# Performance work log

Hardware: AMD Instinct MI355X
Metric: run time of the kernel (lower is better)

The kernel has to match this reference:

```python
import jax, jax.numpy as jnp
import numpy as np

N_TYPES = 4
AEV_DIM = 384
HIDDEN = [160, 128, 96]
CELU_ALPHA = 0.1


def _init_params(key):
    dims = [AEV_DIM] + HIDDEN + [1]
    params = {}
    for li in range(len(dims) - 1):
        key, kw = jax.random.split(key)
        scale = 1.0 / np.sqrt(dims[li])
        # stacked over the N_TYPES per-atom-type experts
        params[f"W{li}"] = (jax.random.normal(kw, (N_TYPES, dims[li], dims[li + 1]), dtype=jnp.float32) * scale)
        params[f"b{li}"] = jnp.zeros((N_TYPES, dims[li + 1]), dtype=jnp.float32)
    return params


def setup_inputs() -> dict:
    key = jax.random.key(0)
    k1, k2, k3 = jax.random.split(key, 3)
    B, A = 2048, 64
    species = jax.random.randint(k1, (B, A), 0, N_TYPES, dtype=jnp.int64)
    aev = jax.random.normal(k2, (B, A, AEV_DIM), dtype=jnp.float32)
    inp = {"species": species, "aev": aev}
    inp.update(_init_params(k3))
    return inp


def _mlp(x, t, W0, b0, W1, b1, W2, b2, W3, b3):
    # x: [N, aev_dim] -> [N] per-atom energy for atom type t
    h = jax.nn.celu(x @ W0[t] + b0[t], alpha=CELU_ALPHA)
    h = jax.nn.celu(h @ W1[t] + b1[t], alpha=CELU_ALPHA)
    h = jax.nn.celu(h @ W2[t] + b2[t], alpha=CELU_ALPHA)
    return (h @ W3[t] + b3[t]).reshape(-1)


def reference(species, aev, W0, b0, W1, b1, W2, b2, W3, b3):
    B, A = species.shape
    sp = species.reshape(-1)            # [B*A]
    x = aev.reshape(-1, aev.shape[-1])  # [B*A, aev_dim]
    out = jnp.zeros(sp.shape, dtype=aev.dtype)  # padding_fill = 0
    for t in range(N_TYPES):  # fixed small expert set
        y = _mlp(x, t, W0, b0, W1, b1, W2, b2, W3, b3)
        out = jnp.where(sp == t, y, out)
    energies = out.reshape(B, A).sum(axis=1)  # reduce over atoms
    return species, energies
```

## Files before the change

### kernel.cpp

```cpp
#include <hip/hip_runtime.h>
#include <math.h>


#define NATOMS   131072
#define NMOL     2048
#define AEV      384
#define NTYPES   4
#define MBLK     128
#define PADTOT   (NATOMS + NTYPES * MBLK)
#define NBLK_MLP (PADTOT / MBLK)
#define NBLK_H   512

#define WB_L1 61440
#define WB_L2 81920
#define WB_T  94208

typedef __attribute__((ext_vector_type(8))) short bf16x8;
typedef __attribute__((ext_vector_type(4))) float f32x4;
typedef unsigned short ushort;

__device__ __forceinline__ float celu01(float v) {
  return (v > 0.f) ? v : 0.1f * (__expf(v * 10.f) - 1.f);
}
__device__ __forceinline__ ushort f2bf(float x) {
  unsigned u = __float_as_uint(x);
  return (ushort)((u + 0x7FFFu + ((u >> 16) & 1u)) >> 16);
}


__global__ void k_pre(const int* __restrict__ species, float* __restrict__ out,
                      int* __restrict__ perm, int* __restrict__ hist,
                      const float* __restrict__ W0, const float* __restrict__ W1,
                      const float* __restrict__ W2, ushort* __restrict__ WB) {
  const int tid = threadIdx.x, blk = blockIdx.x;
  const int i = blk * 256 + tid;
  perm[i] = -1;
  if (i < NATOMS) out[i] = (float)species[i];
  if (i < NMOL) out[NATOMS + i] = 0.f;

  for (int f = i; f < NTYPES * WB_T; f += PADTOT) {
    const int t = f / WB_T, e0 = f - t * WB_T;
    int base, NT, N;
    const float* W;
    if (e0 < WB_L1)      { base = 0;     NT = 10; N = 160; W = W0 + (size_t)t * AEV * 160; }
    else if (e0 < WB_L2) { base = WB_L1; NT = 8;  N = 128; W = W1 + (size_t)t * 160 * 128; }
    else                 { base = WB_L2; NT = 6;  N = 96;  W = W2 + (size_t)t * 128 * 96; }
    const int e = e0 - base, frag = e >> 9, r = e & 511, lane = r >> 3, j = r & 7;
    const int kt = frag / NT, nt = frag - kt * NT;
    const int k = kt * 32 + ((lane >> 4) << 3) + j, n = nt * 16 + (lane & 15);
    WB[(size_t)t * WB_T + e0] = f2bf(W[k * N + n]);
  }

  if (blk < NBLK_H) {
    const int sp = species[i];
    const int wv = tid >> 6;
    __shared__ int wc[4 * NTYPES];
#pragma unroll
    for (int t = 0; t < NTYPES; ++t) {
      const unsigned long long m = __ballot(sp == t);
      if ((tid & 63) == 0) wc[wv * NTYPES + t] = __popcll(m);
    }
    __syncthreads();
    if (tid < NTYPES)
      hist[tid * NBLK_H + blk] = wc[tid] + wc[4 + tid] + wc[8 + tid] + wc[12 + tid];
  }
}


__global__ void k_scan(const int* __restrict__ hist, int* __restrict__ poff,
                       int* __restrict__ boff) {
  __shared__ int tot[NTYPES], base[NTYPES];
  const int tid = threadIdx.x, wv = tid >> 6, lane = tid & 63;
  int s = 0;
  for (int c = 0; c < 8; ++c) s += hist[wv * NBLK_H + c * 64 + lane];
  for (int off = 32; off; off >>= 1) s += __shfl_down(s, off);
  if (lane == 0) tot[wv] = s;
  __syncthreads();
  if (tid == 0) {
    int acc = 0; poff[0] = 0;
    for (int t = 0; t < NTYPES; ++t) {
      base[t] = acc;
      acc += ((tot[t] + 127) >> 7) << 7;
      poff[t + 1] = acc;
    }
  }
  __syncthreads();
  int carry = base[wv];
  for (int c = 0; c < 8; ++c) {
    const int orig = hist[wv * NBLK_H + c * 64 + lane];
    int v = orig;
    for (int off = 1; off < 64; off <<= 1) {
      const int u = __shfl_up(v, off);
      if (lane >= off) v += u;
    }
    boff[wv * NBLK_H + c * 64 + lane] = carry + v - orig;
    carry += __shfl(v, 63);
  }
}

__global__ void k_scatter(const int* __restrict__ species, const int* __restrict__ boff,
                          int* __restrict__ perm) {
  const int tid = threadIdx.x, blk = blockIdx.x;
  const int i = blk * 256 + tid;
  const int sp = species[i];
  const int wv = tid >> 6;
  __shared__ int wc[4 * NTYPES];
  unsigned long long msel = 0;
#pragma unroll
  for (int t = 0; t < NTYPES; ++t) {
    const unsigned long long m = __ballot(sp == t);
    if ((tid & 63) == 0) wc[wv * NTYPES + t] = __popcll(m);
    if (sp == t) msel = m;
  }
  __syncthreads();
  int woff = 0;
  for (int w = 0; w < wv; ++w) woff += wc[w * NTYPES + sp];
  const int rk = __builtin_amdgcn_mbcnt_hi((unsigned)(msel >> 32),
                 __builtin_amdgcn_mbcnt_lo((unsigned)msel, 0));
  perm[boff[sp * NBLK_H + blk] + woff + rk] = i;
}


__global__ __launch_bounds__(256, 2) void k_mlp(
    const float* __restrict__ aev, const ushort* __restrict__ WB,
    const float* __restrict__ b0, const float* __restrict__ b1,
    const float* __restrict__ b2, const float* __restrict__ b3,
    const float* __restrict__ W3,
    const int* __restrict__ poff, const int* __restrict__ perm,
    float* __restrict__ outE)
{
  __shared__ __align__(16) ushort ARENA[4 * 5376];

  const int tid  = threadIdx.x;
  const int lane = tid & 63;
  const int wv   = __builtin_amdgcn_readfirstlane(tid >> 6);
  const int quad = lane >> 4, l15 = lane & 15;
  const int slot0 = blockIdx.x * MBLK;
  const int wbase = wv * 5376;

  int t_ = (slot0 >= poff[1]) + (slot0 >= poff[2]) + (slot0 >= poff[3]);
  if (t_ > 3) t_ = 3;
  const int t = __builtin_amdgcn_readfirstlane(t_);

  const bf16x8* wb0 = (const bf16x8*)(WB + (size_t)t * WB_T);
  const bf16x8* wb1 = (const bf16x8*)(WB + (size_t)t * WB_T + WB_L1);
  const bf16x8* wb2 = (const bf16x8*)(WB + (size_t)t * WB_T + WB_L2);

  const int a  = lane >> 1, ch = lane & 1;
  const int pa = perm[slot0 + wv * 32 + a];
  const float4* src = (const float4*)(aev + (size_t)(pa < 0 ? 0 : pa) * AEV);

  f32x4 acc0[10], acc1[10];
#pragma unroll
  for (int nt = 0; nt < 10; ++nt) {
    const float b = b0[t * 160 + nt * 16 + l15];
    acc0[nt] = (f32x4){b, b, b, b};
    acc1[nt] = (f32x4){b, b, b, b};
  }
#pragma unroll
  for (int s = 0; s < 6; ++s) {
    float4 f[8];
#pragma unroll
    for (int i = 0; i < 8; ++i) {
      f[i] = src[s * 16 + ch * 8 + i];
      if (pa < 0) f[i] = make_float4(0.f, 0.f, 0.f, 0.f);
    }
    const int wb = wbase + (s & 1) * 2304 + a * 72 + ch * 32;
#pragma unroll
    for (int i = 0; i < 4; ++i) {
      bf16x8 p = {(short)f2bf(f[2*i].x), (short)f2bf(f[2*i].y),
                  (short)f2bf(f[2*i].z), (short)f2bf(f[2*i].w),
                  (short)f2bf(f[2*i+1].x), (short)f2bf(f[2*i+1].y),
                  (short)f2bf(f[2*i+1].z), (short)f2bf(f[2*i+1].w)};
      *(bf16x8*)&ARENA[wb + i * 8] = p;
    }
#pragma unroll
    for (int k2 = 0; k2 < 2; ++k2) {
      const int rb = wbase + (s & 1) * 2304 + k2 * 32 + quad * 8;
      const bf16x8 a0 = *(const bf16x8*)&ARENA[rb + l15 * 72];
      const bf16x8 a1 = *(const bf16x8*)&ARENA[rb + (16 + l15) * 72];
      const int ksg = s * 2 + k2;
#pragma unroll
      for (int nt = 0; nt < 10; ++nt) {
        const bf16x8 bf = wb0[(ksg * 10 + nt) * 64 + lane];
        acc0[nt] = __builtin_amdgcn_mfma_f32_16x16x32_bf16(a0, bf, acc0[nt], 0, 0, 0);
        acc1[nt] = __builtin_amdgcn_mfma_f32_16x16x32_bf16(a1, bf, acc1[nt], 0, 0, 0);
      }
    }
  }
#pragma unroll
  for (int nt = 0; nt < 10; ++nt)
#pragma unroll
    for (int r = 0; r < 4; ++r) {
      ARENA[wbase + (quad * 4 + r) * 168 + nt * 16 + l15]        = f2bf(celu01(acc0[nt][r]));
      ARENA[wbase + (16 + quad * 4 + r) * 168 + nt * 16 + l15]   = f2bf(celu01(acc1[nt][r]));
    }

  f32x4 accB0[8], accB1[8];
#pragma unroll
  for (int nt = 0; nt < 8; ++nt) {
    const float b = b1[t * 128 + nt * 16 + l15];
    accB0[nt] = (f32x4){b, b, b, b};
    accB1[nt] = (f32x4){b, b, b, b};
  }
#pragma unroll
  for (int ks = 0; ks < 5; ++ks) {
    const int rb = wbase + ks * 32 + quad * 8;
    const bf16x8 a0 = *(const bf16x8*)&ARENA[rb + l15 * 168];
    const bf16x8 a1 = *(const bf16x8*)&ARENA[rb + (16 + l15) * 168];
#pragma unroll
    for (int nt = 0; nt < 8; ++nt) {
      const bf16x8 bf = wb1[(ks * 8 + nt) * 64 + lane];
      accB0[nt] = __builtin_amdgcn_mfma_f32_16x16x32_bf16(a0, bf, accB0[nt], 0, 0, 0);
      accB1[nt] = __builtin_amdgcn_mfma_f32_16x16x32_bf16(a1, bf, accB1[nt], 0, 0, 0);
    }
  }
#pragma unroll
  for (int nt = 0; nt < 8; ++nt)
#pragma unroll
    for (int r = 0; r < 4; ++r) {
      ARENA[wbase + (quad * 4 + r) * 136 + nt * 16 + l15]      = f2bf(celu01(accB0[nt][r]));
      ARENA[wbase + (16 + quad * 4 + r) * 136 + nt * 16 + l15] = f2bf(celu01(accB1[nt][r]));
    }

  f32x4 accC0[6], accC1[6];
#pragma unroll
  for (int nt = 0; nt < 6; ++nt) {
    const float b = b2[t * 96 + nt * 16 + l15];
    accC0[nt] = (f32x4){b, b, b, b};
    accC1[nt] = (f32x4){b, b, b, b};
  }
#pragma unroll
  for (int ks = 0; ks < 4; ++ks) {
    const int rb = wbase + ks * 32 + quad * 8;
    const bf16x8 a0 = *(const bf16x8*)&ARENA[rb + l15 * 136];
    const bf16x8 a1 = *(const bf16x8*)&ARENA[rb + (16 + l15) * 136];
#pragma unroll
    for (int nt = 0; nt < 6; ++nt) {
      const bf16x8 bf = wb2[(ks * 6 + nt) * 64 + lane];
      accC0[nt] = __builtin_amdgcn_mfma_f32_16x16x32_bf16(a0, bf, accC0[nt], 0, 0, 0);
      accC1[nt] = __builtin_amdgcn_mfma_f32_16x16x32_bf16(a1, bf, accC1[nt], 0, 0, 0);
    }
  }

  float w3v[6];
#pragma unroll
  for (int nt = 0; nt < 6; ++nt) w3v[nt] = W3[t * 96 + nt * 16 + l15];
  const float b3t = b3[t];

  float pe[2][4];
#pragma unroll
  for (int m = 0; m < 2; ++m)
#pragma unroll
    for (int r = 0; r < 4; ++r) {
      float p = 0.f;
#pragma unroll
      for (int nt = 0; nt < 6; ++nt)
        p = fmaf(celu01(m ? accC1[nt][r] : accC0[nt][r]), w3v[nt], p);
      p += __shfl_xor(p, 1);
      p += __shfl_xor(p, 2);
      p += __shfl_xor(p, 4);
      p += __shfl_xor(p, 8);
      pe[m][r] = p;
    }
  if (l15 == 0) {
#pragma unroll
    for (int m = 0; m < 2; ++m)
#pragma unroll
      for (int r = 0; r < 4; ++r) {
        const int ai = perm[slot0 + wv * 32 + m * 16 + quad * 4 + r];
        if (ai >= 0) atomicAdd(&outE[ai >> 6], pe[m][r] + b3t);
      }
  }
}


extern "C" void kernel_launch(void* const* d_in, const int* in_sizes, int n_in,
                              void* d_out, int out_size, void* d_ws, size_t ws_size,
                              hipStream_t stream)
{
  const int*   species = (const int*)d_in[0];
  const float* aev     = (const float*)d_in[1];
  const float* W0 = (const float*)d_in[2];
  const float* b0 = (const float*)d_in[3];
  const float* W1 = (const float*)d_in[4];
  const float* b1 = (const float*)d_in[5];
  const float* W2 = (const float*)d_in[6];
  const float* b2 = (const float*)d_in[7];
  const float* W3 = (const float*)d_in[8];
  const float* b3 = (const float*)d_in[9];
  float* out = (float*)d_out;

  int* poff = (int*)d_ws;
  int* hist = poff + 8;
  int* boff = hist + NTYPES * NBLK_H;
  int* perm = boff + NTYPES * NBLK_H;
  ushort* WB = (ushort*)(perm + PADTOT);

  k_pre    <<<PADTOT / 256, 256, 0, stream>>>(species, out, perm, hist, W0, W1, W2, WB);
  k_scan   <<<1, 256, 0, stream>>>(hist, poff, boff);
  k_scatter<<<NBLK_H, 256, 0, stream>>>(species, boff, perm);
  k_mlp    <<<NBLK_MLP, 256, 0, stream>>>(aev, WB, b0, b1, b2, b3, W3,
                                          poff, perm, out + NATOMS);
}
```

Baseline: 398.7 us.

## Pre-sort and convert AEV rows to bf16 in scatter kernel, feed MFMA from global

The scatter kernel now also gathers each atom's AEV row into sorted order, converts it to bf16 and writes it into a padded workspace buffer. The MLP kernel then loads layer-0 A fragments straight from that contiguous bf16 buffer, dropping the per-block fp32 gather, conversion and LDS staging. This shortens the MLP's first layer and improves locality, at the cost of an extra bf16 write and read-back of the whole activation matrix. Padding rows in the buffer are no longer zeroed, so correctness relies on the later code masking those slots.

```diff
diff --git a/kernel.cpp b/kernel.cpp
--- a/kernel.cpp
+++ b/kernel.cpp
@@ -98,12 +98,14 @@
   }
 }
 
-__global__ void k_scatter(const int* __restrict__ species, const int* __restrict__ boff,
-                          int* __restrict__ perm) {
+
+__global__ void k_sortcvt(const int* __restrict__ species, const float* __restrict__ aev,
+                          const int* __restrict__ boff, int* __restrict__ perm,
+                          ushort* __restrict__ Xs) {
   const int tid = threadIdx.x, blk = blockIdx.x;
   const int i = blk * 256 + tid;
   const int sp = species[i];
-  const int wv = tid >> 6;
+  const int wv = tid >> 6, lane = tid & 63;
   __shared__ int wc[4 * NTYPES];
   unsigned long long msel = 0;
 #pragma unroll
@@ -117,12 +119,28 @@
   for (int w = 0; w < wv; ++w) woff += wc[w * NTYPES + sp];
   const int rk = __builtin_amdgcn_mbcnt_hi((unsigned)(msel >> 32),
                  __builtin_amdgcn_mbcnt_lo((unsigned)msel, 0));
-  perm[boff[sp * NBLK_H + blk] + woff + rk] = i;
+  const int dst = boff[sp * NBLK_H + blk] + woff + rk;
+  perm[dst] = i;
+
+  const int sub = lane >> 4, c = lane & 15;
+  for (int g = 0; g < 16; ++g) {
+    const int src = __shfl(i,   g * 4 + sub);
+    const int dR  = __shfl(dst, g * 4 + sub);
+    const float4* s4 = (const float4*)(aev + (size_t)src * AEV);
+    ushort* dp = Xs + (size_t)dR * AEV;
+#pragma unroll
+    for (int itc = 0; itc < 6; ++itc) {
+      const int c4 = c + itc * 16;
+      const float4 v = s4[c4];
+      ushort4 p = {f2bf(v.x), f2bf(v.y), f2bf(v.z), f2bf(v.w)};
+      *(ushort4*)(dp + c4 * 4) = p;
+    }
+  }
 }
 
 
 __global__ __launch_bounds__(256, 2) void k_mlp(
-    const float* __restrict__ aev, const ushort* __restrict__ WB,
+    const ushort* __restrict__ Xs, const ushort* __restrict__ WB,
     const float* __restrict__ b0, const float* __restrict__ b1,
     const float* __restrict__ b2, const float* __restrict__ b3,
     const float* __restrict__ W3,
@@ -146,9 +164,7 @@
   const bf16x8* wb1 = (const bf16x8*)(WB + (size_t)t * WB_T + WB_L1);
   const bf16x8* wb2 = (const bf16x8*)(WB + (size_t)t * WB_T + WB_L2);
 
-  const int a  = lane >> 1, ch = lane & 1;
-  const int pa = perm[slot0 + wv * 32 + a];
-  const float4* src = (const float4*)(aev + (size_t)(pa < 0 ? 0 : pa) * AEV);
+  const ushort* XsW = Xs + (size_t)(slot0 + wv * 32) * AEV;
 
   f32x4 acc0[10], acc1[10];
 #pragma unroll
@@ -158,42 +174,22 @@
     acc1[nt] = (f32x4){b, b, b, b};
   }
 #pragma unroll
-  for (int s = 0; s < 6; ++s) {
-    float4 f[8];
-#pragma unroll
-    for (int i = 0; i < 8; ++i) {
-      f[i] = src[s * 16 + ch * 8 + i];
-      if (pa < 0) f[i] = make_float4(0.f, 0.f, 0.f, 0.f);
-    }
-    const int wb = wbase + (s & 1) * 2304 + a * 72 + ch * 32;
-#pragma unroll
-    for (int i = 0; i < 4; ++i) {
-      bf16x8 p = {(short)f2bf(f[2*i].x), (short)f2bf(f[2*i].y),
-                  (short)f2bf(f[2*i].z), (short)f2bf(f[2*i].w),
-                  (short)f2bf(f[2*i+1].x), (short)f2bf(f[2*i+1].y),
-                  (short)f2bf(f[2*i+1].z), (short)f2bf(f[2*i+1].w)};
-      *(bf16x8*)&ARENA[wb + i * 8] = p;
-    }
-#pragma unroll
-    for (int k2 = 0; k2 < 2; ++k2) {
-      const int rb = wbase + (s & 1) * 2304 + k2 * 32 + quad * 8;
-      const bf16x8 a0 = *(const bf16x8*)&ARENA[rb + l15 * 72];
-      const bf16x8 a1 = *(const bf16x8*)&ARENA[rb + (16 + l15) * 72];
-      const int ksg = s * 2 + k2;
-#pragma unroll
-      for (int nt = 0; nt < 10; ++nt) {
-        const bf16x8 bf = wb0[(ksg * 10 + nt) * 64 + lane];
-        acc0[nt] = __builtin_amdgcn_mfma_f32_16x16x32_bf16(a0, bf, acc0[nt], 0, 0, 0);
-        acc1[nt] = __builtin_amdgcn_mfma_f32_16x16x32_bf16(a1, bf, acc1[nt], 0, 0, 0);
-      }
+  for (int s = 0; s < 12; ++s) {
+    const bf16x8 a0 = *(const bf16x8*)(XsW + l15 * AEV + s * 32 + quad * 8);
+    const bf16x8 a1 = *(const bf16x8*)(XsW + (16 + l15) * AEV + s * 32 + quad * 8);
+#pragma unroll
+    for (int nt = 0; nt < 10; ++nt) {
+      const bf16x8 bf = wb0[(s * 10 + nt) * 64 + lane];
+      acc0[nt] = __builtin_amdgcn_mfma_f32_16x16x32_bf16(a0, bf, acc0[nt], 0, 0, 0);
+      acc1[nt] = __builtin_amdgcn_mfma_f32_16x16x32_bf16(a1, bf, acc1[nt], 0, 0, 0);
     }
   }
 #pragma unroll
   for (int nt = 0; nt < 10; ++nt)
 #pragma unroll
     for (int r = 0; r < 4; ++r) {
-      ARENA[wbase + (quad * 4 + r) * 168 + nt * 16 + l15]        = f2bf(celu01(acc0[nt][r]));
-      ARENA[wbase + (16 + quad * 4 + r) * 168 + nt * 16 + l15]   = f2bf(celu01(acc1[nt][r]));
+      ARENA[wbase + (quad * 4 + r) * 168 + nt * 16 + l15]      = f2bf(celu01(acc0[nt][r]));
+      ARENA[wbase + (16 + quad * 4 + r) * 168 + nt * 16 + l15] = f2bf(celu01(acc1[nt][r]));
     }
 
   f32x4 accB0[8], accB1[8];
@@ -295,11 +291,12 @@
   int* hist = poff + 8;
   int* boff = hist + NTYPES * NBLK_H;
   int* perm = boff + NTYPES * NBLK_H;
-  ushort* WB = (ushort*)(perm + PADTOT);
+  ushort* Xs = (ushort*)(perm + PADTOT);
+  ushort* WB = Xs + (size_t)PADTOT * AEV;
 
   k_pre    <<<PADTOT / 256, 256, 0, stream>>>(species, out, perm, hist, W0, W1, W2, WB);
   k_scan   <<<1, 256, 0, stream>>>(hist, poff, boff);
-  k_scatter<<<NBLK_H, 256, 0, stream>>>(species, boff, perm);
-  k_mlp    <<<NBLK_MLP, 256, 0, stream>>>(aev, WB, b0, b1, b2, b3, W3,
+  k_sortcvt<<<NATOMS / 256, 256, 0, stream>>>(species, aev, boff, perm, Xs);
+  k_mlp    <<<NBLK_MLP, 256, 0, stream>>>(Xs, WB, b0, b1, b2, b3, W3,
                                           poff, perm, out + NATOMS);
 }
```

Result: slower. 502.9 us (+26.1%).
